# Kernel tuning notes

Hardware: AMD Instinct MI355X
Metric: run time of the kernel (lower is better)

The kernel has to match this reference:

```python
import jax, jax.numpy as jnp
import numpy as np

Z_RES, N_RES = 128, 512
M_PTS = 2_000_000


def trilinear_devoxelize(grid, coords):
    """Gather-based trilinear interpolation.
    grid:   (Z, N, N, C) voxel grid
    coords: (M, 3) float positions in voxel index space (z, x, y)
    returns (M, C)
    """
    Zd, Nd = grid.shape[0], grid.shape[1]
    c0f = jnp.floor(coords)
    frac = coords - c0f                      # (M, 3) fractional offsets
    maxi = jnp.array([Zd - 1, Nd - 1, Nd - 1], dtype=jnp.int32)
    c0 = jnp.clip(c0f.astype(jnp.int32), 0, maxi)
    c1 = jnp.clip(c0 + 1, 0, maxi)
    fz, fx, fy = frac[:, 0:1], frac[:, 1:2], frac[:, 2:3]
    gz, gx, gy = 1.0 - fz, 1.0 - fx, 1.0 - fy

    def g(zi, xi, yi):
        return grid[zi, xi, yi]              # (M, C) gather

    out = (g(c0[:, 0], c0[:, 1], c0[:, 2]) * gz * gx * gy
         + g(c0[:, 0], c0[:, 1], c1[:, 2]) * gz * gx * fy
         + g(c0[:, 0], c1[:, 1], c0[:, 2]) * gz * fx * gy
         + g(c0[:, 0], c1[:, 1], c1[:, 2]) * gz * fx * fy
         + g(c1[:, 0], c0[:, 1], c0[:, 2]) * fz * gx * gy
         + g(c1[:, 0], c0[:, 1], c1[:, 2]) * fz * gx * fy
         + g(c1[:, 0], c1[:, 1], c0[:, 2]) * fz * fx * gy
         + g(c1[:, 0], c1[:, 1], c1[:, 2]) * fz * fx * fy)
    return out


def setup_inputs() -> dict:
    key = jax.random.key(0)
    k1, k2 = jax.random.split(key)
    extents = jnp.array([Z_RES - 1, N_RES - 1, N_RES - 1], jnp.float32)
    coords = jax.random.uniform(k1, (M_PTS, 3), dtype=jnp.float32) * extents
    # init_scale = 1.0 -> albedo ~ U[0,1); normal initialized to zeros (per module)
    albedo = jax.random.uniform(k2, (Z_RES, N_RES, N_RES), dtype=jnp.float32)
    normal = jnp.zeros((Z_RES, N_RES, N_RES, 3), dtype=jnp.float32)
    return {"coords": coords, "albedo": albedo, "normal": normal}


def reference(coords, albedo, normal):
    base_normal = jnp.array([-1.0, 0.0, 0.0], dtype=jnp.float32)
    a = trilinear_devoxelize(albedo[..., None], coords)[:, 0]   # (M,)
    n = trilinear_devoxelize(normal, coords)                    # (M, 3)
    a = jax.nn.elu(a)
    n = jnp.tanh(n) + base_normal
    # F.normalize(dim=1, eps=1e-12): divide by max(||n||, eps)
    norm = jnp.maximum(jnp.linalg.norm(n, axis=1, keepdims=True), 1e-12)
    n = n / norm
    return (a, n)
```

## Files before the change

kernel.cpp:

```cpp
#include <hip/hip_runtime.h>
#include <math.h>

#define ZR 128
#define NR 512

typedef unsigned int u32x4 __attribute__((ext_vector_type(4)));
typedef unsigned short u16x8 __attribute__((ext_vector_type(8)));
typedef unsigned long long u64x2v __attribute__((ext_vector_type(2)));


__device__ __forceinline__ float bf16_to_f32(unsigned short u) {
    return __uint_as_float(((unsigned int)u) << 16);
}

__device__ __forceinline__ unsigned short f32_to_bf16_rne(float v) {
    unsigned int u = __float_as_uint(v);
    return (unsigned short)((u + 0x7FFFu + ((u >> 16) & 1u)) >> 16);
}

__device__ __forceinline__ float extract_bf16(u64x2v v, int yo) {
    unsigned long long w = (yo & 4) ? v.y : v.x;
    unsigned int sh = ((unsigned)yo & 3u) << 4;
    return bf16_to_f32((unsigned short)(w >> sh));
}

__device__ __forceinline__ void zcheck_range(
    const u32x4* __restrict__ normal4, long long lo, long long hi,
    long long rank, long long nthreads, unsigned int* __restrict__ flag)
{
    unsigned int acc = 0;
    long long i = lo + rank * 256 + threadIdx.x;
    for (; i + nthreads < hi; i += 2 * nthreads) {
        u32x4 v0 = __builtin_nontemporal_load(&normal4[i]);
        u32x4 v1 = __builtin_nontemporal_load(&normal4[i + nthreads]);
        acc |= v0.x | v0.y | v0.z | v0.w | v1.x | v1.y | v1.z | v1.w;
    }
    if (i < hi) {
        u32x4 v = __builtin_nontemporal_load(&normal4[i]);
        acc |= v.x | v.y | v.z | v.w;
    }
    if (__ballot(acc != 0) && ((threadIdx.x & 63) == 0))
        atomicOr(flag, 1u);
}

__device__ __forceinline__ float interp_rows(
    const unsigned short* __restrict__ tiled,
    float cz, float cx, float cy)
{
    float fz0 = floorf(cz), fx0 = floorf(cx), fy0 = floorf(cy);
    float fz = cz - fz0, fx = cx - fx0, fy = cy - fy0;

    int z0 = min(max((int)fz0, 0), ZR - 1);
    int x0 = min(max((int)fx0, 0), NR - 1);
    int y0 = min(max((int)fy0, 0), NR - 1);
    int z1 = min(z0 + 1, ZR - 1);
    int x1 = min(x0 + 1, NR - 1);
    int y1 = min(y0 + 1, NR - 1);

    float gz = 1.0f - fz, gx = 1.0f - fx, gy = 1.0f - fy;

    float w000 = gz * gx * gy, w001 = gz * gx * fy;
    float w010 = gz * fx * gy, w011 = gz * fx * fy;
    float w100 = fz * gx * gy, w101 = fz * gx * fy;
    float w110 = fz * fx * gy, w111 = fz * fx * fy;

    int xo0 = (x0 & 3) << 3, xo1 = (x1 & 3) << 3;
    int yo0 = y0 & 7,        yo1 = y1 & 7;
    int c0 = (y0 >> 3) << 5, c1 = (y1 >> 3) << 5;
    int r00 = ((z0 << 7) + (x0 >> 2)) << 11;
    int r01 = ((z0 << 7) + (x1 >> 2)) << 11;
    int r10 = ((z1 << 7) + (x0 >> 2)) << 11;
    int r11 = ((z1 << 7) + (x1 >> 2)) << 11;

    const u64x2v* base = (const u64x2v*)tiled;

    u64x2v vA = base[(r00 + c0 + xo0) >> 3];
    u64x2v vB = base[(r01 + c0 + xo1) >> 3];
    u64x2v vC = base[(r10 + c0 + xo0) >> 3];
    u64x2v vD = base[(r11 + c0 + xo1) >> 3];

    u64x2v vA2 = vA, vB2 = vB, vC2 = vC, vD2 = vD;
    if (c1 != c0) {
        vA2 = base[(r00 + c1 + xo0) >> 3];
        vB2 = base[(r01 + c1 + xo1) >> 3];
        vC2 = base[(r10 + c1 + xo0) >> 3];
        vD2 = base[(r11 + c1 + xo1) >> 3];
    }

    return
        extract_bf16(vA,  yo0) * w000 + extract_bf16(vA2, yo1) * w001 +
        extract_bf16(vB,  yo0) * w010 + extract_bf16(vB2, yo1) * w011 +
        extract_bf16(vC,  yo0) * w100 + extract_bf16(vC2, yo1) * w101 +
        extract_bf16(vD,  yo0) * w110 + extract_bf16(vD2, yo1) * w111;
}

__global__ __launch_bounds__(256) void repack_zcheck_kernel(
    const float* __restrict__ albedo,
    unsigned short* __restrict__ tiled,
    const u32x4* __restrict__ normal4,
    unsigned int* __restrict__ flag,
    long long n4h)
{
    unsigned int b = blockIdx.x;
    if (b < 4096u) {
        zcheck_range(normal4, 0, n4h, (long long)b, 4096LL * 256, flag);
        return;
    }
    unsigned int b2 = b - 4096u;
    int z = (int)(b2 >> 7);
    int xt = (int)(b2 & 127u);

    __shared__ float s[2048];
    const u32x4* src = (const u32x4*)(albedo + ((size_t)z * NR + (size_t)xt * 4) * NR);
    for (int k = threadIdx.x; k < 512; k += 256) {
        u32x4 v = __builtin_nontemporal_load(&src[k]);
        ((u32x4*)s)[k] = v;
    }
    __syncthreads();

    unsigned short* dst = tiled + (size_t)b2 * 2048;
    int t8 = threadIdx.x * 8;
    u16x8 outv;
#pragma unroll
    for (int j = 0; j < 8; j++) {
        int k = t8 + j;
        int yt = k >> 5;
        int r = k & 31;
        int xr = r >> 3;
        int yy = r & 7;
        outv[j] = f32_to_bf16_rne(s[xr * 512 + (yt << 3) + yy]);
    }
    *(u16x8*)(dst + t8) = outv;
}

#define K2_ZBLK 1536
__global__ __launch_bounds__(256) void interp_zcheck_kernel(
    const float* __restrict__ coords,
    const unsigned short* __restrict__ tiled,
    const u32x4* __restrict__ normal4,
    const unsigned int* __restrict__ normal_tail,
    int tail_cnt,
    unsigned int* __restrict__ flag,
    float* __restrict__ out_a,
    float* __restrict__ out_n,
    int M, long long n4h, long long n4)
{
    unsigned int b = blockIdx.x;
    if (b < K2_ZBLK) {
        if (b == 0 && threadIdx.x < (unsigned)tail_cnt) {
            unsigned int tv = normal_tail[threadIdx.x];
            if (tv) atomicOr(flag, 1u);
        }
        zcheck_range(normal4, n4h, n4, (long long)b, (long long)K2_ZBLK * 256, flag);
        return;
    }
    int t = (int)(b - K2_ZBLK) * 256 + threadIdx.x;
    int i0 = t * 2;
    if (i0 >= M) return;

    const float2* cp = (const float2*)(coords + (size_t)i0 * 3);
    float2 q0 = cp[0], q1 = cp[1], q2 = cp[2];

    float a0 = interp_rows(tiled, q0.x, q0.y, q1.x);
    a0 = (a0 > 0.0f) ? a0 : expm1f(a0);

    float2* on = (float2*)(out_n + (size_t)i0 * 3);
    if (i0 + 1 < M) {
        float a1 = interp_rows(tiled, q1.y, q2.x, q2.y);
        a1 = (a1 > 0.0f) ? a1 : expm1f(a1);
        *(float2*)(out_a + i0) = make_float2(a0, a1);
        on[0] = make_float2(-1.0f, 0.0f);
        on[1] = make_float2(0.0f, -1.0f);
        on[2] = make_float2(0.0f, 0.0f);
    } else {
        out_a[i0] = a0;
        out_n[3 * i0 + 0] = -1.0f;
        out_n[3 * i0 + 1] = 0.0f;
        out_n[3 * i0 + 2] = 0.0f;
    }
}

__global__ __launch_bounds__(256) void normal_full_kernel(
    const float* __restrict__ coords,
    const float* __restrict__ normal,
    const unsigned int* __restrict__ flag,
    float* __restrict__ out_n,
    int M)
{
    if (*flag == 0) return;

    int stride = gridDim.x * 256;
    for (int i = blockIdx.x * 256 + threadIdx.x; i < M; i += stride) {
        float cz = coords[3 * i + 0];
        float cx = coords[3 * i + 1];
        float cy = coords[3 * i + 2];

        float fz0 = floorf(cz), fx0 = floorf(cx), fy0 = floorf(cy);
        float fz = cz - fz0, fx = cx - fx0, fy = cy - fy0;

        int z0 = min(max((int)fz0, 0), ZR - 1);
        int x0 = min(max((int)fx0, 0), NR - 1);
        int y0 = min(max((int)fy0, 0), NR - 1);
        int z1 = min(z0 + 1, ZR - 1);
        int x1 = min(x0 + 1, NR - 1);
        int y1 = min(y0 + 1, NR - 1);

        float gz = 1.0f - fz, gx = 1.0f - fx, gy = 1.0f - fy;

        float w000 = gz * gx * gy, w001 = gz * gx * fy;
        float w010 = gz * fx * gy, w011 = gz * fx * fy;
        float w100 = fz * gx * gy, w101 = fz * gx * fy;
        float w110 = fz * fx * gy, w111 = fz * fx * fy;

        size_t b00 = ((size_t)z0 * NR + x0) * NR;
        size_t b01 = ((size_t)z0 * NR + x1) * NR;
        size_t b10 = ((size_t)z1 * NR + x0) * NR;
        size_t b11 = ((size_t)z1 * NR + x1) * NR;

        float n0 = 0.0f, n1 = 0.0f, n2 = 0.0f;
#define ACC(base, yy, w)                                           \
        {                                                          \
            const float* qp = normal + ((base) + (size_t)(yy)) * 3;\
            n0 += qp[0] * (w);                                     \
            n1 += qp[1] * (w);                                     \
            n2 += qp[2] * (w);                                     \
        }
        ACC(b00, y0, w000); ACC(b00, y1, w001);
        ACC(b01, y0, w010); ACC(b01, y1, w011);
        ACC(b10, y0, w100); ACC(b10, y1, w101);
        ACC(b11, y0, w110); ACC(b11, y1, w111);
#undef ACC

        n0 = tanhf(n0) - 1.0f;
        n1 = tanhf(n1);
        n2 = tanhf(n2);

        float nrm = sqrtf(n0 * n0 + n1 * n1 + n2 * n2);
        nrm = fmaxf(nrm, 1e-12f);
        float inv = 1.0f / nrm;

        out_n[3 * i + 0] = n0 * inv;
        out_n[3 * i + 1] = n1 * inv;
        out_n[3 * i + 2] = n2 * inv;
    }
}

__global__ __launch_bounds__(256) void devox_direct(
    const float* __restrict__ coords,
    const float* __restrict__ albedo,
    const float* __restrict__ normal,
    float* __restrict__ out_a,
    float* __restrict__ out_n,
    int M)
{
    int i = blockIdx.x * 256 + threadIdx.x;
    if (i >= M) return;

    float cz = coords[3 * i + 0];
    float cx = coords[3 * i + 1];
    float cy = coords[3 * i + 2];

    float fz0 = floorf(cz), fx0 = floorf(cx), fy0 = floorf(cy);
    float fz = cz - fz0, fx = cx - fx0, fy = cy - fy0;

    int z0 = min(max((int)fz0, 0), ZR - 1);
    int x0 = min(max((int)fx0, 0), NR - 1);
    int y0 = min(max((int)fy0, 0), NR - 1);
    int z1 = min(z0 + 1, ZR - 1);
    int x1 = min(x0 + 1, NR - 1);
    int y1 = min(y0 + 1, NR - 1);

    float gz = 1.0f - fz, gx = 1.0f - fx, gy = 1.0f - fy;
    float w000 = gz * gx * gy, w001 = gz * gx * fy;
    float w010 = gz * fx * gy, w011 = gz * fx * fy;
    float w100 = fz * gx * gy, w101 = fz * gx * fy;
    float w110 = fz * fx * gy, w111 = fz * fx * fy;

    size_t b00 = ((size_t)z0 * NR + x0) * NR;
    size_t b01 = ((size_t)z0 * NR + x1) * NR;
    size_t b10 = ((size_t)z1 * NR + x0) * NR;
    size_t b11 = ((size_t)z1 * NR + x1) * NR;

    float a =
        albedo[b00 + y0] * w000 + albedo[b00 + y1] * w001 +
        albedo[b01 + y0] * w010 + albedo[b01 + y1] * w011 +
        albedo[b10 + y0] * w100 + albedo[b10 + y1] * w101 +
        albedo[b11 + y0] * w110 + albedo[b11 + y1] * w111;

    float n0 = 0.0f, n1 = 0.0f, n2 = 0.0f;
#define ACC(base, yy, w)                                           \
    {                                                              \
        const float* qp = normal + ((base) + (size_t)(yy)) * 3;    \
        n0 += qp[0] * (w);                                         \
        n1 += qp[1] * (w);                                         \
        n2 += qp[2] * (w);                                         \
    }
    ACC(b00, y0, w000); ACC(b00, y1, w001);
    ACC(b01, y0, w010); ACC(b01, y1, w011);
    ACC(b10, y0, w100); ACC(b10, y1, w101);
    ACC(b11, y0, w110); ACC(b11, y1, w111);
#undef ACC

    a = (a > 0.0f) ? a : expm1f(a);
    n0 = tanhf(n0) - 1.0f;
    n1 = tanhf(n1);
    n2 = tanhf(n2);
    float nrm = sqrtf(n0 * n0 + n1 * n1 + n2 * n2);
    nrm = fmaxf(nrm, 1e-12f);
    float inv = 1.0f / nrm;

    out_a[i] = a;
    out_n[3 * i + 0] = n0 * inv;
    out_n[3 * i + 1] = n1 * inv;
    out_n[3 * i + 2] = n2 * inv;
}

extern "C" void kernel_launch(void* const* d_in, const int* in_sizes, int n_in,
                              void* d_out, int out_size, void* d_ws, size_t ws_size,
                              hipStream_t stream) {
    const float* coords = (const float*)d_in[0];
    const float* albedo = (const float*)d_in[1];
    const float* normal = (const float*)d_in[2];

    int M = in_sizes[0] / 3;
    long long normal_elems = (long long)in_sizes[2];
    long long n4 = normal_elems / 4;
    long long n4h = n4 / 2;
    int tail_cnt = (int)(normal_elems & 3);
    const unsigned int* normal_tail = (const unsigned int*)normal + n4 * 4;

    float* out = (float*)d_out;
    float* out_a = out;
    float* out_n = out + M;

    size_t tiled_off = 256;
    size_t tiled_bytes = (size_t)128 * 128 * 64 * 32 * 2;
    if (ws_size < tiled_off + tiled_bytes) {
        int nblk = (M + 255) / 256;
        devox_direct<<<nblk, 256, 0, stream>>>(coords, albedo, normal, out_a, out_n, M);
        return;
    }

    unsigned int* flag = (unsigned int*)d_ws;
    unsigned short* tiled = (unsigned short*)((char*)d_ws + tiled_off);

    (void)hipMemsetAsync(flag, 0, sizeof(unsigned int), stream);

    repack_zcheck_kernel<<<4096 + 16384, 256, 0, stream>>>(
        albedo, tiled, (const u32x4*)normal, flag, n4h);

    int iblk = (M + 511) / 512;
    interp_zcheck_kernel<<<K2_ZBLK + iblk, 256, 0, stream>>>(
        coords, tiled, (const u32x4*)normal, normal_tail, tail_cnt,
        flag, out_a, out_n, M, n4h, n4);

    normal_full_kernel<<<2048, 256, 0, stream>>>(coords, normal, flag, out_n, M);
}
```

Baseline: 681.6 us.

## Move normal zero-check and default normal fill into repack kernel, slim interp

Moves the whole normal-grid zero check and the default-normal output fill into the first kernel, alongside the albedo bf16 repack. The interpolation kernel then handles one point per thread and writes only the albedo output, using nontemporal stores. The aim is to overlap the bandwidth-bound zero scan and output fill with the repack, and to shorten the gather kernel. The cost is a heavier first kernel that now reads the entire normal grid while also repacking albedo.

```diff
diff --git a/kernel.cpp b/kernel.cpp
--- a/kernel.cpp
+++ b/kernel.cpp
@@ -3,6 +3,7 @@
 
 #define ZR 128
 #define NR 512
+#define ZB1 4096
 
 typedef unsigned int u32x4 __attribute__((ext_vector_type(4)));
 typedef unsigned short u16x8 __attribute__((ext_vector_type(8)));
@@ -94,90 +95,91 @@
         extract_bf16(vD,  yo0) * w110 + extract_bf16(vD2, yo1) * w111;
 }
 
-__global__ __launch_bounds__(256) void repack_zcheck_kernel(
+__global__ __launch_bounds__(256) void phase1_kernel(
     const float* __restrict__ albedo,
     unsigned short* __restrict__ tiled,
     const u32x4* __restrict__ normal4,
+    const unsigned int* __restrict__ normal_tail, int tail_cnt,
     unsigned int* __restrict__ flag,
-    long long n4h)
+    float* __restrict__ out_n,
+    long long n4, int M, int FB)
 {
     unsigned int b = blockIdx.x;
-    if (b < 4096u) {
-        zcheck_range(normal4, 0, n4h, (long long)b, 4096LL * 256, flag);
+
+    if (b < (unsigned)ZB1) {
+        if (b == 0 && threadIdx.x < (unsigned)tail_cnt) {
+            if (normal_tail[threadIdx.x]) atomicOr(flag, 1u);
+        }
+        zcheck_range(normal4, 0, n4, (long long)b, (long long)ZB1 * 256, flag);
         return;
     }
-    unsigned int b2 = b - 4096u;
-    int z = (int)(b2 >> 7);
-    int xt = (int)(b2 & 127u);
-
-    __shared__ float s[2048];
-    const u32x4* src = (const u32x4*)(albedo + ((size_t)z * NR + (size_t)xt * 4) * NR);
-    for (int k = threadIdx.x; k < 512; k += 256) {
-        u32x4 v = __builtin_nontemporal_load(&src[k]);
-        ((u32x4*)s)[k] = v;
-    }
-    __syncthreads();
-
-    unsigned short* dst = tiled + (size_t)b2 * 2048;
-    int t8 = threadIdx.x * 8;
-    u16x8 outv;
+    b -= (unsigned)ZB1;
+
+    if (b < 16384u) {
+        int z = (int)(b >> 7);
+        int xt = (int)(b & 127u);
+
+        __shared__ float s[2048];
+        const u32x4* src = (const u32x4*)(albedo + ((size_t)z * NR + (size_t)xt * 4) * NR);
+        for (int k = threadIdx.x; k < 512; k += 256) {
+            u32x4 v = __builtin_nontemporal_load(&src[k]);
+            ((u32x4*)s)[k] = v;
+        }
+        __syncthreads();
+
+        unsigned short* dst = tiled + (size_t)b * 2048;
+        int t8 = threadIdx.x * 8;
+        u16x8 outv;
 #pragma unroll
-    for (int j = 0; j < 8; j++) {
-        int k = t8 + j;
-        int yt = k >> 5;
-        int r = k & 31;
-        int xr = r >> 3;
-        int yy = r & 7;
-        outv[j] = f32_to_bf16_rne(s[xr * 512 + (yt << 3) + yy]);
-    }
-    *(u16x8*)(dst + t8) = outv;
-}
-
-#define K2_ZBLK 1536
-__global__ __launch_bounds__(256) void interp_zcheck_kernel(
+        for (int j = 0; j < 8; j++) {
+            int k = t8 + j;
+            int yt = k >> 5;
+            int r = k & 31;
+            int xr = r >> 3;
+            int yy = r & 7;
+            outv[j] = f32_to_bf16_rne(s[xr * 512 + (yt << 3) + yy]);
+        }
+        *(u16x8*)(dst + t8) = outv;
+        return;
+    }
+    b -= 16384u;
+
+    long long total = 3LL * M;
+    if ((M & 3) == 0) {
+        long long f4 = (long long)b * 256 + threadIdx.x;
+        long long nf4 = total >> 2;
+        if (f4 < nf4) {
+            const unsigned int B = 0xBF800000u;
+            int rmod = (int)(f4 % 3);
+            u32x4 v;
+            if (rmod == 0)      v = (u32x4){B, 0u, 0u, B};
+            else if (rmod == 1) v = (u32x4){0u, 0u, B, 0u};
+            else                v = (u32x4){0u, B, 0u, 0u};
+            __builtin_nontemporal_store(v, &((u32x4*)out_n)[f4]);
+        }
+    } else {
+        long long stride = (long long)FB * 256;
+        for (long long qq = (long long)b * 256 + threadIdx.x; qq < total; qq += stride)
+            out_n[qq] = ((qq % 3) == 0) ? -1.0f : 0.0f;
+    }
+}
+
+__global__ __launch_bounds__(256) void interp_kernel(
     const float* __restrict__ coords,
     const unsigned short* __restrict__ tiled,
-    const u32x4* __restrict__ normal4,
-    const unsigned int* __restrict__ normal_tail,
-    int tail_cnt,
-    unsigned int* __restrict__ flag,
     float* __restrict__ out_a,
-    float* __restrict__ out_n,
-    int M, long long n4h, long long n4)
-{
-    unsigned int b = blockIdx.x;
-    if (b < K2_ZBLK) {
-        if (b == 0 && threadIdx.x < (unsigned)tail_cnt) {
-            unsigned int tv = normal_tail[threadIdx.x];
-            if (tv) atomicOr(flag, 1u);
-        }
-        zcheck_range(normal4, n4h, n4, (long long)b, (long long)K2_ZBLK * 256, flag);
-        return;
-    }
-    int t = (int)(b - K2_ZBLK) * 256 + threadIdx.x;
-    int i0 = t * 2;
-    if (i0 >= M) return;
-
-    const float2* cp = (const float2*)(coords + (size_t)i0 * 3);
-    float2 q0 = cp[0], q1 = cp[1], q2 = cp[2];
-
-    float a0 = interp_rows(tiled, q0.x, q0.y, q1.x);
-    a0 = (a0 > 0.0f) ? a0 : expm1f(a0);
-
-    float2* on = (float2*)(out_n + (size_t)i0 * 3);
-    if (i0 + 1 < M) {
-        float a1 = interp_rows(tiled, q1.y, q2.x, q2.y);
-        a1 = (a1 > 0.0f) ? a1 : expm1f(a1);
-        *(float2*)(out_a + i0) = make_float2(a0, a1);
-        on[0] = make_float2(-1.0f, 0.0f);
-        on[1] = make_float2(0.0f, -1.0f);
-        on[2] = make_float2(0.0f, 0.0f);
-    } else {
-        out_a[i0] = a0;
-        out_n[3 * i0 + 0] = -1.0f;
-        out_n[3 * i0 + 1] = 0.0f;
-        out_n[3 * i0 + 2] = 0.0f;
-    }
+    int M)
+{
+    int i = blockIdx.x * 256 + threadIdx.x;
+    if (i >= M) return;
+
+    float cz = coords[3 * i + 0];
+    float cx = coords[3 * i + 1];
+    float cy = coords[3 * i + 2];
+
+    float a = interp_rows(tiled, cz, cx, cy);
+    a = (a > 0.0f) ? a : expm1f(a);
+    __builtin_nontemporal_store(a, &out_a[i]);
 }
 
 __global__ __launch_bounds__(256) void normal_full_kernel(
@@ -325,7 +327,6 @@
     int M = in_sizes[0] / 3;
     long long normal_elems = (long long)in_sizes[2];
     long long n4 = normal_elems / 4;
-    long long n4h = n4 / 2;
     int tail_cnt = (int)(normal_elems & 3);
     const unsigned int* normal_tail = (const unsigned int*)normal + n4 * 4;
 
@@ -346,13 +347,15 @@
 
     (void)hipMemsetAsync(flag, 0, sizeof(unsigned int), stream);
 
-    repack_zcheck_kernel<<<4096 + 16384, 256, 0, stream>>>(
-        albedo, tiled, (const u32x4*)normal, flag, n4h);
-
-    int iblk = (M + 511) / 512;
-    interp_zcheck_kernel<<<K2_ZBLK + iblk, 256, 0, stream>>>(
-        coords, tiled, (const u32x4*)normal, normal_tail, tail_cnt,
-        flag, out_a, out_n, M, n4h, n4);
+    long long total_n = 3LL * M;
+    int FB = ((M & 3) == 0) ? (int)((total_n / 4 + 255) / 256) : 2048;
+    if (FB < 1) FB = 1;
+    phase1_kernel<<<ZB1 + 16384 + FB, 256, 0, stream>>>(
+        albedo, tiled, (const u32x4*)normal, normal_tail, tail_cnt,
+        flag, out_n, n4, M, FB);
+
+    int iblk = (M + 255) / 256;
+    interp_kernel<<<iblk, 256, 0, stream>>>(coords, tiled, out_a, M);
 
     normal_full_kernel<<<2048, 256, 0, stream>>>(coords, normal, flag, out_n, M);
 }
```

Result: no change. 681.8 us (+0.0%).
